# Optimization experiments

Measured on AMD Instinct MI355X. Metric: run time of the kernel, lower is better.

## Reference

```python
import jax, jax.numpy as jnp
import numpy as np

DIM = 192; H = 6; HD = DIM // H; WS = 8; N = WS * WS; B = 2048; NW = 64
SCALE = HD ** -0.5


def _rel_idx():
    # replicates torch meshgrid (indexing='ij') relative position index
    coords = np.stack(np.meshgrid(np.arange(WS), np.arange(WS), indexing='ij'))  # [2,WS,WS]
    flat = coords.reshape(2, -1)  # [2, N]
    rel = flat[:, :, None] - flat[:, None, :]  # [2, N, N]
    rel = rel.transpose(1, 2, 0).astype(np.int64)
    rel[..., 0] += WS - 1
    rel[..., 1] += WS - 1
    rel[..., 0] *= 2 * WS - 1
    return jnp.asarray(rel.sum(-1), dtype=jnp.int32)  # [N, N]


def setup_inputs() -> dict:
    key = jax.random.key(0)
    ks = jax.random.split(key, 8)
    x1 = jax.random.normal(ks[0], (B, N, DIM), jnp.float32)
    x2 = jax.random.normal(ks[1], (B, N, DIM), jnp.float32)
    mask = jnp.zeros((NW, N, N), jnp.float32)
    qw = jax.random.normal(ks[2], (DIM, DIM), jnp.float32) * 0.02
    qb = jnp.zeros((DIM,), jnp.float32)
    kvw = jax.random.normal(ks[3], (2 * DIM, DIM), jnp.float32) * 0.02
    kvb = jnp.zeros((2 * DIM,), jnp.float32)
    rpb = jax.random.normal(ks[4], ((2 * WS - 1) * (2 * WS - 1), H), jnp.float32) * 0.02
    gamma = jnp.full((1,), 0.5, jnp.float32)  # nonzero to exercise LAM path
    pw = jax.random.normal(ks[5], (DIM, DIM), jnp.float32) * 0.02
    pb = jnp.zeros((DIM,), jnp.float32)
    rel_idx = _rel_idx()
    return {"x1": x1, "x2": x2, "mask": mask, "qw": qw, "qb": qb, "kvw": kvw,
            "kvb": kvb, "rpb": rpb, "gamma": gamma, "pw": pw, "pb": pb,
            "rel_idx": rel_idx}


def reference(x1, x2, mask, qw, qb, kvw, kvb, rpb, gamma, pw, pb, rel_idx):
    # q projection -> [B, H, N, HD], pre-scaled (torch code reassigns q = q*scale)
    q = (x1 @ qw.T + qb).reshape(B, N, H, HD).transpose(0, 2, 1, 3) * SCALE
    kv = (x2 @ kvw.T + kvb).reshape(B, N, 2, H, HD)
    k = kv[:, :, 0].transpose(0, 2, 1, 3)  # [B, H, N, HD]
    v = kv[:, :, 1].transpose(0, 2, 1, 3)
    attn = jnp.einsum('bhnd,bhmd->bhnm', q, k)  # [B, H, N, N]
    # gathered relative position bias [H, N, N]
    bias = rpb[rel_idx.reshape(-1)].reshape(N, N, H).transpose(2, 0, 1)
    attn = attn + bias[None]
    attn = attn.reshape(B // NW, NW, H, N, N) + mask[None, :, None]
    attn = jax.nn.softmax(attn.reshape(B, H, N, N), axis=-1)
    y = jnp.einsum('bhnm,bhmd->bhnd', attn, v)  # [B, H, N, HD]
    # LAM module: channel-wise (dim) attention over (head*num)
    xp = y.transpose(0, 3, 1, 2)              # [B, HD, H, N]
    flat = xp.reshape(B, HD, H * N)
    energy = jnp.einsum('bik,bjk->bij', flat, flat)  # [B, HD, HD]
    # note: original computes energy_new but softmaxes raw energy; replicate
    att = jax.nn.softmax(energy, axis=-1)
    out = jnp.einsum('bij,bjk->bik', att, flat).reshape(B, HD, H, N)
    out = gamma * out + xp
    lam = out.transpose(0, 2, 3, 1)            # [B, H, N, HD]
    x = (lam.transpose(0, 2, 1, 3).reshape(B, N, DIM)
         + q.transpose(0, 2, 1, 3).reshape(B, N, DIM)
         + x1)
    return x @ pw.T + pb
```

## Files before the change

### kernel.cpp

```cpp
#include <hip/hip_runtime.h>

#define DIM 192
#define NTOK 64
#define NHEAD 6
#define HDIM 32
#define SCALE 0.17677669529663687f

typedef __attribute__((ext_vector_type(8))) short bf16x8;
typedef __attribute__((ext_vector_type(4))) float f32x4;

__device__ __forceinline__ ushort f2bf(float f) {
    union { float f; unsigned u; } x; x.f = f;
    unsigned r = x.u + 0x7FFFu + ((x.u >> 16) & 1u);
    return (ushort)(r >> 16);
}
__device__ __forceinline__ float bf2f(ushort h) {
    union { unsigned u; float f; } x; x.u = ((unsigned)h) << 16;
    return x.f;
}

__device__ __forceinline__ f32x4 MF(bf16x8 a, bf16x8 b, f32x4 c) {
    return __builtin_amdgcn_mfma_f32_16x16x32_bf16(a, b, c, 0, 0, 0);
}

__device__ __forceinline__ bf16x8 frag(const ushort* base, int stride, int r0, int k0) {
    const int l = threadIdx.x & 63;
    return *(const bf16x8*)(base + (r0 + (l & 15)) * stride + (k0 + ((l >> 4) << 3)));
}

__global__ void prep_weights(const float* __restrict__ qw, const float* __restrict__ kvw,
                             const float* __restrict__ pw, ushort* __restrict__ wbf) {
    int i = blockIdx.x * 256 + threadIdx.x;
    if (i < 36864) wbf[i] = f2bf(qw[i]);
    else if (i < 110592) wbf[i] = f2bf(kvw[i - 36864]);
    else if (i < 147456) wbf[i] = f2bf(pw[i - 110592]);
}

__global__ void prep_cmb(const float* __restrict__ rpb, const float* __restrict__ mask,
                         ushort* __restrict__ cmb) {
    int t = blockIdx.x * 256 + threadIdx.x;
    int e = t << 2;
    int n0 = e & 63;
    int m  = (e >> 6) & 63;
    int hw = e >> 12;
    int h = hw % 6, w = hw / 6;
#pragma unroll
    for (int j = 0; j < 4; ++j) {
        int n = n0 + j;
        int ridx = ((n >> 3) - (m >> 3) + 7) * 15 + ((n & 7) - (m & 7) + 7);
        float v = rpb[ridx * 6 + h] + mask[(w * 64 + n) * 64 + m];
        cmb[e + j] = f2bf(v);
    }
}

__global__ __launch_bounds__(256, 3) void proj_qkv(
    const float* __restrict__ x1, const float* __restrict__ x2,
    const float* __restrict__ qb, const float* __restrict__ kvb,
    const ushort* __restrict__ qwbf, const ushort* __restrict__ kvwbf,
    ushort* __restrict__ Qf, ushort* __restrict__ Kf, ushort* __restrict__ Vf)
{
    __shared__ __align__(16) ushort sXA[64 * 200];
    __shared__ __align__(16) ushort stg[4 * 2560];
    const int tid = threadIdx.x, wave = tid >> 6, lane = tid & 63;
    const int g = lane >> 4, mcol = lane & 15;
    const int b = blockIdx.x >> 1;
    const int kind = blockIdx.x & 1;
    ushort* st = stg + wave * 2560;

    {
        const float4* src = (const float4*)((kind ? x1 : x2) + (size_t)b * 12288);
        for (int i = tid; i < 3072; i += 256) {
            float4 v = src[i];
            int e = i << 2; int n = e / DIM; int c = e - n * DIM;
            ushort4 w;
            ((ushort*)&w)[0] = f2bf(v.x); ((ushort*)&w)[1] = f2bf(v.y);
            ((ushort*)&w)[2] = f2bf(v.z); ((ushort*)&w)[3] = f2bf(v.w);
            *(ushort4*)(&sXA[n * 200 + c]) = w;
        }
    }
    __syncthreads();

    if (kind == 0) {
        for (int t = wave; t < 12; t += 4) {
            const int isV = (t >= 6) ? 1 : 0;
            const int h = isV ? (t - 6) : t;
            bf16x8 wf[2][6];
#pragma unroll
            for (int c2 = 0; c2 < 2; ++c2) {
                int ctg = (isV ? (12 + 2 * h) : (2 * h)) + c2;
#pragma unroll
                for (int ks = 0; ks < 6; ++ks)
                    wf[c2][ks] = frag(kvwbf, DIM, ctg * 16, ks * 32);
            }
            f32x4 acc[4][2];
#pragma unroll
            for (int rt = 0; rt < 4; ++rt)
#pragma unroll
                for (int c2 = 0; c2 < 2; ++c2) acc[rt][c2] = (f32x4){0.f, 0.f, 0.f, 0.f};
#pragma unroll
            for (int rt = 0; rt < 4; ++rt) {
                bf16x8 af[6];
#pragma unroll
                for (int ks = 0; ks < 6; ++ks) af[ks] = frag(sXA, 200, rt * 16, ks * 32);
#pragma unroll
                for (int c2 = 0; c2 < 2; ++c2)
#pragma unroll
                    for (int ks = 0; ks < 6; ++ks)
                        acc[rt][c2] = MF(af[ks], wf[c2][ks], acc[rt][c2]);
            }
            if (!isV) {
#pragma unroll
                for (int c2 = 0; c2 < 2; ++c2) {
                    float bv = kvb[h * 32 + c2 * 16 + mcol];
#pragma unroll
                    for (int rt = 0; rt < 4; ++rt)
#pragma unroll
                        for (int j = 0; j < 4; ++j)
                            st[(rt * 16 + (g << 2) + j) * 40 + c2 * 16 + mcol] = f2bf(acc[rt][c2][j] + bv);
                }
                asm volatile("s_waitcnt lgkmcnt(0)" ::: "memory");
#pragma unroll
                for (int ct = 0; ct < 4; ++ct) {
                    bf16x8 fr = frag(st, 40, ct * 16, 0);
                    *(bf16x8*)(Kf + ((size_t)(b * 6 + h) * 4 + ct) * 512 + lane * 8) = fr;
                }
                asm volatile("s_waitcnt lgkmcnt(0)" ::: "memory");
            } else {
#pragma unroll
                for (int c2 = 0; c2 < 2; ++c2) {
                    float bv = kvb[192 + h * 32 + c2 * 16 + mcol];
#pragma unroll
                    for (int rt = 0; rt < 4; ++rt) {
                        ushort4 w4;
#pragma unroll
                        for (int j = 0; j < 4; ++j) ((ushort*)&w4)[j] = f2bf(acc[rt][c2][j] + bv);
                        *(ushort4*)(&st[(c2 * 16 + mcol) * 72 + rt * 16 + (g << 2)]) = w4;
                    }
                }
                asm volatile("s_waitcnt lgkmcnt(0)" ::: "memory");
#pragma unroll
                for (int c = 0; c < 2; ++c)
#pragma unroll
                    for (int ctd = 0; ctd < 2; ++ctd) {
                        bf16x8 fr = frag(st, 72, ctd * 16, c * 32);
                        *(bf16x8*)(Vf + (((size_t)(b * 6 + h) * 2 + c) * 2 + ctd) * 512 + lane * 8) = fr;
                    }
                asm volatile("s_waitcnt lgkmcnt(0)" ::: "memory");
            }
        }
    } else {
        for (int t = wave; t < 6; t += 4) {
            const int h = t;
            bf16x8 wf[2][6];
#pragma unroll
            for (int c2 = 0; c2 < 2; ++c2)
#pragma unroll
                for (int ks = 0; ks < 6; ++ks)
                    wf[c2][ks] = frag(qwbf, DIM, (2 * h + c2) * 16, ks * 32);
            f32x4 acc[4][2];
#pragma unroll
            for (int rt = 0; rt < 4; ++rt)
#pragma unroll
                for (int c2 = 0; c2 < 2; ++c2) acc[rt][c2] = (f32x4){0.f, 0.f, 0.f, 0.f};
#pragma unroll
            for (int rt = 0; rt < 4; ++rt) {
                bf16x8 af[6];
#pragma unroll
                for (int ks = 0; ks < 6; ++ks) af[ks] = frag(sXA, 200, rt * 16, ks * 32);
#pragma unroll
                for (int c2 = 0; c2 < 2; ++c2)
#pragma unroll
                    for (int ks = 0; ks < 6; ++ks)
                        acc[rt][c2] = MF(af[ks], wf[c2][ks], acc[rt][c2]);
            }
#pragma unroll
            for (int c2 = 0; c2 < 2; ++c2) {
                float bv = qb[h * 32 + c2 * 16 + mcol];
#pragma unroll
                for (int rt = 0; rt < 4; ++rt)
#pragma unroll
                    for (int j = 0; j < 4; ++j)
                        st[(rt * 16 + (g << 2) + j) * 40 + c2 * 16 + mcol] =
                            f2bf((acc[rt][c2][j] + bv) * SCALE);
            }
            asm volatile("s_waitcnt lgkmcnt(0)" ::: "memory");
#pragma unroll
            for (int rt = 0; rt < 4; ++rt) {
                bf16x8 fr = frag(st, 40, rt * 16, 0);
                *(bf16x8*)(Qf + ((size_t)(b * 6 + h) * 4 + rt) * 512 + lane * 8) = fr;
            }
            asm volatile("s_waitcnt lgkmcnt(0)" ::: "memory");
        }
    }
}

__global__ __launch_bounds__(256, 4) void attn_heads(
    const ushort* __restrict__ Qf, ushort* KfY,
    const ushort* __restrict__ Vf, const ushort* __restrict__ cmb)
{
    __shared__ __align__(16) ushort sP[4 * 1280];
    const int tid = threadIdx.x, wave = tid >> 6, lane = tid & 63;
    const int g = lane >> 4, mcol = lane & 15;
    const int gid = blockIdx.x * 4 + wave;
    const int w = gid / 6, h = gid - 6 * (gid / 6);
    const f32x4 zero4 = {0.f, 0.f, 0.f, 0.f};

    const ushort* qp = Qf  + (size_t)gid * 2048;
    ushort*       kp = KfY + (size_t)gid * 2048;
    const ushort* vp = Vf  + (size_t)gid * 2048;
    const ushort* cp = cmb + (size_t)((w & 63) * 6 + h) * 4096;
    ushort* slot = sP + wave * 1280;

    bf16x8 kb[4], vb[4];
#pragma unroll
    for (int ct = 0; ct < 4; ++ct) kb[ct] = *(const bf16x8*)(kp + ct * 512 + lane * 8);
#pragma unroll
    for (int c = 0; c < 4; ++c) vb[c] = *(const bf16x8*)(vp + c * 512 + lane * 8);

    ushort4 y4[4][2];
#pragma unroll
    for (int rt = 0; rt < 4; ++rt) {
        bf16x8 qa = *(const bf16x8*)(qp + rt * 512 + lane * 8);
        f32x4 acc[4];
#pragma unroll
        for (int ct = 0; ct < 4; ++ct) acc[ct] = MF(qa, kb[ct], zero4);
#pragma unroll
        for (int ct = 0; ct < 4; ++ct) {
            ushort4 b4 = *(const ushort4*)(cp + (ct * 16 + mcol) * 64 + rt * 16 + (g << 2));
#pragma unroll
            for (int j = 0; j < 4; ++j) acc[ct][j] += bf2f(((ushort*)&b4)[j]);
        }
        float sm[4];
#pragma unroll
        for (int j = 0; j < 4; ++j) {
            float v = fmaxf(fmaxf(acc[0][j], acc[1][j]), fmaxf(acc[2][j], acc[3][j]));
            v = fmaxf(v, __shfl_xor(v, 1, 64));
            v = fmaxf(v, __shfl_xor(v, 2, 64));
            v = fmaxf(v, __shfl_xor(v, 4, 64));
            v = fmaxf(v, __shfl_xor(v, 8, 64));
            float s = 0.f;
#pragma unroll
            for (int ct = 0; ct < 4; ++ct) {
                float p = __expf(acc[ct][j] - v);
                acc[ct][j] = p; s += p;
            }
            s += __shfl_xor(s, 1, 64);
            s += __shfl_xor(s, 2, 64);
            s += __shfl_xor(s, 4, 64);
            s += __shfl_xor(s, 8, 64);
            sm[j] = 1.0f / s;
        }
#pragma unroll
        for (int ct = 0; ct < 4; ++ct)
#pragma unroll
            for (int j = 0; j < 4; ++j)
                slot[((g << 2) + j) * 72 + ct * 16 + mcol] = f2bf(acc[ct][j] * sm[j]);
        asm volatile("s_waitcnt lgkmcnt(0)" ::: "memory");
        f32x4 ay0 = zero4, ay1 = zero4;
#pragma unroll
        for (int c = 0; c < 2; ++c) {
            bf16x8 pa = frag(slot, 72, 0, c * 32);
            ay0 = MF(pa, vb[c * 2 + 0], ay0);
            ay1 = MF(pa, vb[c * 2 + 1], ay1);
        }
        asm volatile("s_waitcnt lgkmcnt(0)" ::: "memory");
#pragma unroll
        for (int j = 0; j < 4; ++j) {
            ((ushort*)&y4[rt][0])[j] = f2bf(ay0[j]);
            ((ushort*)&y4[rt][1])[j] = f2bf(ay1[j]);
        }
    }
#pragma unroll
    for (int rt = 0; rt < 4; ++rt)
#pragma unroll
        for (int ctd = 0; ctd < 2; ++ctd)
            *(ushort4*)(kp + (ctd * 16 + mcol) * 64 + rt * 16 + (g << 2)) = y4[rt][ctd];
}

__global__ __launch_bounds__(256, 4) void lam_proj(
    const ushort* __restrict__ Yd, const ushort* __restrict__ Qf,
    const float* __restrict__ x1, const float* __restrict__ gammap,
    const ushort* __restrict__ pwbf, const float* __restrict__ pb,
    float* __restrict__ out)
{
    __shared__ __align__(16) ushort sYF[13824];
    __shared__ __align__(16) float  sE[32 * 33];
    __shared__ __align__(16) ushort sAtt[32 * 40];

    const int tid = threadIdx.x, wave = tid >> 6, lane = tid & 63;
    const int g = lane >> 4, mcol = lane & 15;
    const int b = blockIdx.x;
    const float gamma = gammap[0];
    const f32x4 zero4 = {0.f, 0.f, 0.f, 0.f};

    {
        const ushort* src = Yd + (size_t)b * 12288;
        for (int i = tid; i < 3072; i += 256) {
            int hd = i >> 9;
            int rem = i & 511;
            int row = rem >> 4, k4 = rem & 15;
            ushort4 v = *(const ushort4*)(src + hd * 2048 + row * 64 + k4 * 4);
            *(ushort4*)(&sYF[hd * 2304 + row * 72 + k4 * 4]) = v;
        }
    }
    __syncthreads();

    {
        int rt = wave >> 1, ct = wave & 1;
        f32x4 a0 = zero4, a1 = zero4;
#pragma unroll
        for (int hd = 0; hd < 6; hd += 2) {
            const ushort* Y0 = sYF + hd * 2304;
            const ushort* Y1 = sYF + (hd + 1) * 2304;
#pragma unroll
            for (int kk = 0; kk < 2; ++kk) {
                a0 = MF(frag(Y0, 72, rt * 16, kk * 32), frag(Y0, 72, ct * 16, kk * 32), a0);
                a1 = MF(frag(Y1, 72, rt * 16, kk * 32), frag(Y1, 72, ct * 16, kk * 32), a1);
            }
        }
        f32x4 acc = a0 + a1;
#pragma unroll
        for (int j = 0; j < 4; ++j)
            sE[(rt * 16 + (g << 2) + j) * 33 + ct * 16 + mcol] = acc[j];
    }
    __syncthreads();

    {
        int r = tid >> 3, l8 = tid & 7;
        float e[4];
        float mx = -1e30f;
#pragma unroll
        for (int k = 0; k < 4; ++k) { e[k] = sE[r * 33 + l8 + k * 8]; mx = fmaxf(mx, e[k]); }
        mx = fmaxf(mx, __shfl_xor(mx, 1, 64));
        mx = fmaxf(mx, __shfl_xor(mx, 2, 64));
        mx = fmaxf(mx, __shfl_xor(mx, 4, 64));
        float s = 0.f;
#pragma unroll
        for (int k = 0; k < 4; ++k) { e[k] = __expf(e[k] - mx); s += e[k]; }
        s += __shfl_xor(s, 1, 64);
        s += __shfl_xor(s, 2, 64);
        s += __shfl_xor(s, 4, 64);
        float rs = 1.0f / s;
#pragma unroll
        for (int k = 0; k < 4; ++k) sAtt[r * 40 + l8 + k * 8] = f2bf(e[k] * rs);
    }
    __syncthreads();

    ushort4 w4st[12];
#pragma unroll
    for (int i = 0; i < 12; ++i) {
        int t = wave + i * 4;
        int rtL = t & 1, ct = t >> 1;
        int col = ct * 16 + mcol;
        int hh = col >> 6, nn = col & 63;
        const ushort* Yh = sYF + hh * 2304;
        bf16x8 aa = frag(sAtt, 40, rtL * 16, 0);
        bf16x8 bb;
#pragma unroll
        for (int jj = 0; jj < 8; ++jj) bb[jj] = (short)Yh[((g << 3) + jj) * 72 + nn];
        f32x4 acc = MF(aa, bb, zero4);
        int d0 = rtL * 16 + (g << 2);
        ushort4 qv4 = *(const ushort4*)(Qf + (size_t)(b * 6 + hh) * 2048 +
                                        (nn >> 4) * 512 + ((nn & 15) + ((d0 >> 3) << 4)) * 8 + (d0 & 7));
        float4 xv4 = *(const float4*)(x1 + (size_t)b * 12288 + nn * 192 + hh * 32 + d0);
        ushort4 w4;
#pragma unroll
        for (int j = 0; j < 4; ++j) {
            float flatv = bf2f(Yh[(d0 + j) * 72 + nn]);
            float val = gamma * acc[j] + flatv + bf2f(((ushort*)&qv4)[j]) + ((const float*)&xv4)[j];
            ((ushort*)&w4)[j] = f2bf(val);
        }
        w4st[i] = w4;
    }
    __syncthreads();
#pragma unroll
    for (int i = 0; i < 12; ++i) {
        int t = wave + i * 4;
        int rtL = t & 1, ct = t >> 1;
        int col = ct * 16 + mcol;
        int hh = col >> 6, nn = col & 63;
        int d0 = rtL * 16 + (g << 2);
        *(ushort4*)(&sYF[nn * 200 + hh * 32 + d0]) = w4st[i];
    }
    __syncthreads();

    {
        float* outp = out + (size_t)b * 12288;
        const int rt = wave;
        bf16x8 af[6];
#pragma unroll
        for (int ks = 0; ks < 6; ++ks) af[ks] = frag(sYF, 200, rt * 16, ks * 32);
        for (int ct = 0; ct < 12; ++ct) {
            f32x4 acc = zero4;
#pragma unroll
            for (int ks = 0; ks < 6; ++ks)
                acc = MF(af[ks], frag(pwbf, DIM, ct * 16, ks * 32), acc);
            int co = ct * 16 + mcol;
            float pbv = pb[co];
#pragma unroll
            for (int j = 0; j < 4; ++j)
                outp[(rt * 16 + (g << 2) + j) * DIM + co] = acc[j] + pbv;
        }
    }
}

extern "C" void kernel_launch(void* const* d_in, const int* in_sizes, int n_in,
                              void* d_out, int out_size, void* d_ws, size_t ws_size,
                              hipStream_t stream) {
    const float* x1    = (const float*)d_in[0];
    const float* x2    = (const float*)d_in[1];
    const float* mask  = (const float*)d_in[2];
    const float* qw    = (const float*)d_in[3];
    const float* qbv   = (const float*)d_in[4];
    const float* kvw   = (const float*)d_in[5];
    const float* kvbv  = (const float*)d_in[6];
    const float* rpb   = (const float*)d_in[7];
    const float* gamma = (const float*)d_in[8];
    const float* pw    = (const float*)d_in[9];
    const float* pbv   = (const float*)d_in[10];
    ushort* wbf = (ushort*)d_ws;

    prep_weights<<<576, 256, 0, stream>>>(qw, kvw, pw, wbf);

    ushort* cmb = wbf + 147456;
    ushort* Qf  = wbf + 1720320;
    ushort* Kf  = wbf + 26886144;
    ushort* Vf  = wbf + 52051968;
    prep_cmb<<<1536, 256, 0, stream>>>(rpb, mask, cmb);
    proj_qkv<<<4096, 256, 0, stream>>>(x1, x2, qbv, kvbv,
                                       wbf, wbf + 36864, Qf, Kf, Vf);
    attn_heads<<<3072, 256, 0, stream>>>(Qf, Kf, Vf, cmb);
    lam_proj<<<2048, 256, 0, stream>>>(Kf, Qf, x1, gamma,
                                       wbf + 110592, pbv, (float*)d_out);
}
```

Baseline: 296.6 us.

## Switch Q/KV intermediates to row-major layout and tile projection over two batches

```diff
diff --git a/kernel.cpp b/kernel.cpp
--- a/kernel.cpp
+++ b/kernel.cpp
@@ -53,174 +53,120 @@
     }
 }
 
-__global__ __launch_bounds__(256, 3) void proj_qkv(
+__global__ __launch_bounds__(256, 3) void proj2(
     const float* __restrict__ x1, const float* __restrict__ x2,
     const float* __restrict__ qb, const float* __restrict__ kvb,
     const ushort* __restrict__ qwbf, const ushort* __restrict__ kvwbf,
-    ushort* __restrict__ Qf, ushort* __restrict__ Kf, ushort* __restrict__ Vf)
+    ushort* __restrict__ Qb, ushort* __restrict__ KVb)
 {
-    __shared__ __align__(16) ushort sXA[64 * 200];
-    __shared__ __align__(16) ushort stg[4 * 2560];
+    __shared__ __align__(16) ushort sX[128 * 200];
     const int tid = threadIdx.x, wave = tid >> 6, lane = tid & 63;
     const int g = lane >> 4, mcol = lane & 15;
-    const int b = blockIdx.x >> 1;
-    const int kind = blockIdx.x & 1;
-    ushort* st = stg + wave * 2560;
-
-    {
-        const float4* src = (const float4*)((kind ? x1 : x2) + (size_t)b * 12288);
-        for (int i = tid; i < 3072; i += 256) {
+    const int isQ = (blockIdx.x >= 1024);
+    const int grp = isQ ? (blockIdx.x - 1024) : blockIdx.x;
+    const f32x4 zero4 = {0.f, 0.f, 0.f, 0.f};
+
+    {
+        const float4* src = (const float4*)((isQ ? x1 : x2) + (size_t)grp * 24576);
+        for (int i = tid; i < 6144; i += 256) {
             float4 v = src[i];
             int e = i << 2; int n = e / DIM; int c = e - n * DIM;
             ushort4 w;
             ((ushort*)&w)[0] = f2bf(v.x); ((ushort*)&w)[1] = f2bf(v.y);
             ((ushort*)&w)[2] = f2bf(v.z); ((ushort*)&w)[3] = f2bf(v.w);
-            *(ushort4*)(&sXA[n * 200 + c]) = w;
-        }
-    }
-    __syncthreads();
-
-    if (kind == 0) {
-        for (int t = wave; t < 12; t += 4) {
-            const int isV = (t >= 6) ? 1 : 0;
-            const int h = isV ? (t - 6) : t;
-            bf16x8 wf[2][6];
-#pragma unroll
-            for (int c2 = 0; c2 < 2; ++c2) {
-                int ctg = (isV ? (12 + 2 * h) : (2 * h)) + c2;
+            *(ushort4*)(&sX[n * 200 + c]) = w;
+        }
+    }
+    __syncthreads();
+
+    const size_t grow = (size_t)grp * 128;
+    if (!isQ) {
+        for (int q = 0; q < 6; ++q) {
+            int ct = wave * 6 + q;
+            bf16x8 wf[6];
+#pragma unroll
+            for (int ks = 0; ks < 6; ++ks) wf[ks] = frag(kvwbf, DIM, ct * 16, ks * 32);
+            int co = ct * 16 + mcol;
+            float bv = kvb[co];
+            for (int rt = 0; rt < 8; ++rt) {
+                f32x4 acc = zero4;
 #pragma unroll
                 for (int ks = 0; ks < 6; ++ks)
-                    wf[c2][ks] = frag(kvwbf, DIM, ctg * 16, ks * 32);
+                    acc = MF(frag(sX, 200, rt * 16, ks * 32), wf[ks], acc);
+#pragma unroll
+                for (int j = 0; j < 4; ++j)
+                    KVb[(grow + rt * 16 + (g << 2) + j) * 384 + co] = f2bf(acc[j] + bv);
             }
-            f32x4 acc[4][2];
-#pragma unroll
-            for (int rt = 0; rt < 4; ++rt)
-#pragma unroll
-                for (int c2 = 0; c2 < 2; ++c2) acc[rt][c2] = (f32x4){0.f, 0.f, 0.f, 0.f};
-#pragma unroll
-            for (int rt = 0; rt < 4; ++rt) {
-                bf16x8 af[6];
-#pragma unroll
-                for (int ks = 0; ks < 6; ++ks) af[ks] = frag(sXA, 200, rt * 16, ks * 32);
-#pragma unroll
-                for (int c2 = 0; c2 < 2; ++c2)
-#pragma unroll
-                    for (int ks = 0; ks < 6; ++ks)
-                        acc[rt][c2] = MF(af[ks], wf[c2][ks], acc[rt][c2]);
+        }
+    } else {
+        for (int q = 0; q < 3; ++q) {
+            int ct = wave * 3 + q;
+            bf16x8 wf[6];
+#pragma unroll
+            for (int ks = 0; ks < 6; ++ks) wf[ks] = frag(qwbf, DIM, ct * 16, ks * 32);
+            int co = ct * 16 + mcol;
+            float bv = qb[co];
+            for (int rt = 0; rt < 8; ++rt) {
+                f32x4 acc = zero4;
+#pragma unroll
+                for (int ks = 0; ks < 6; ++ks)
+                    acc = MF(frag(sX, 200, rt * 16, ks * 32), wf[ks], acc);
+#pragma unroll
+                for (int j = 0; j < 4; ++j)
+                    Qb[(grow + rt * 16 + (g << 2) + j) * DIM + co] = f2bf((acc[j] + bv) * SCALE);
             }
-            if (!isV) {
-#pragma unroll
-                for (int c2 = 0; c2 < 2; ++c2) {
-                    float bv = kvb[h * 32 + c2 * 16 + mcol];
-#pragma unroll
-                    for (int rt = 0; rt < 4; ++rt)
-#pragma unroll
-                        for (int j = 0; j < 4; ++j)
-                            st[(rt * 16 + (g << 2) + j) * 40 + c2 * 16 + mcol] = f2bf(acc[rt][c2][j] + bv);
-                }
-                asm volatile("s_waitcnt lgkmcnt(0)" ::: "memory");
-#pragma unroll
-                for (int ct = 0; ct < 4; ++ct) {
-                    bf16x8 fr = frag(st, 40, ct * 16, 0);
-                    *(bf16x8*)(Kf + ((size_t)(b * 6 + h) * 4 + ct) * 512 + lane * 8) = fr;
-                }
-                asm volatile("s_waitcnt lgkmcnt(0)" ::: "memory");
-            } else {
-#pragma unroll
-                for (int c2 = 0; c2 < 2; ++c2) {
-                    float bv = kvb[192 + h * 32 + c2 * 16 + mcol];
-#pragma unroll
-                    for (int rt = 0; rt < 4; ++rt) {
-                        ushort4 w4;
-#pragma unroll
-                        for (int j = 0; j < 4; ++j) ((ushort*)&w4)[j] = f2bf(acc[rt][c2][j] + bv);
-                        *(ushort4*)(&st[(c2 * 16 + mcol) * 72 + rt * 16 + (g << 2)]) = w4;
-                    }
-                }
-                asm volatile("s_waitcnt lgkmcnt(0)" ::: "memory");
-#pragma unroll
-                for (int c = 0; c < 2; ++c)
-#pragma unroll
-                    for (int ctd = 0; ctd < 2; ++ctd) {
-                        bf16x8 fr = frag(st, 72, ctd * 16, c * 32);
-                        *(bf16x8*)(Vf + (((size_t)(b * 6 + h) * 2 + c) * 2 + ctd) * 512 + lane * 8) = fr;
-                    }
-                asm volatile("s_waitcnt lgkmcnt(0)" ::: "memory");
-            }
-        }
-    } else {
-        for (int t = wave; t < 6; t += 4) {
-            const int h = t;
-            bf16x8 wf[2][6];
-#pragma unroll
-            for (int c2 = 0; c2 < 2; ++c2)
-#pragma unroll
-                for (int ks = 0; ks < 6; ++ks)
-                    wf[c2][ks] = frag(qwbf, DIM, (2 * h + c2) * 16, ks * 32);
-            f32x4 acc[4][2];
-#pragma unroll
-            for (int rt = 0; rt < 4; ++rt)
-#pragma unroll
-                for (int c2 = 0; c2 < 2; ++c2) acc[rt][c2] = (f32x4){0.f, 0.f, 0.f, 0.f};
-#pragma unroll
-            for (int rt = 0; rt < 4; ++rt) {
-                bf16x8 af[6];
-#pragma unroll
-                for (int ks = 0; ks < 6; ++ks) af[ks] = frag(sXA, 200, rt * 16, ks * 32);
-#pragma unroll
-                for (int c2 = 0; c2 < 2; ++c2)
-#pragma unroll
-                    for (int ks = 0; ks < 6; ++ks)
-                        acc[rt][c2] = MF(af[ks], wf[c2][ks], acc[rt][c2]);
-            }
-#pragma unroll
-            for (int c2 = 0; c2 < 2; ++c2) {
-                float bv = qb[h * 32 + c2 * 16 + mcol];
-#pragma unroll
-                for (int rt = 0; rt < 4; ++rt)
-#pragma unroll
-                    for (int j = 0; j < 4; ++j)
-                        st[(rt * 16 + (g << 2) + j) * 40 + c2 * 16 + mcol] =
-                            f2bf((acc[rt][c2][j] + bv) * SCALE);
-            }
-            asm volatile("s_waitcnt lgkmcnt(0)" ::: "memory");
-#pragma unroll
-            for (int rt = 0; rt < 4; ++rt) {
-                bf16x8 fr = frag(st, 40, rt * 16, 0);
-                *(bf16x8*)(Qf + ((size_t)(b * 6 + h) * 4 + rt) * 512 + lane * 8) = fr;
-            }
-            asm volatile("s_waitcnt lgkmcnt(0)" ::: "memory");
-        }
-    }
-}
-
-__global__ __launch_bounds__(256, 4) void attn_heads(
-    const ushort* __restrict__ Qf, ushort* KfY,
-    const ushort* __restrict__ Vf, const ushort* __restrict__ cmb)
+        }
+    }
+}
+
+__global__ __launch_bounds__(256, 5) void attn_heads(
+    const ushort* __restrict__ Qb, ushort* __restrict__ KVb,
+    const ushort* __restrict__ cmb)
 {
     __shared__ __align__(16) ushort sP[4 * 1280];
+    __shared__ __align__(16) ushort sV[4 * 2176];
     const int tid = threadIdx.x, wave = tid >> 6, lane = tid & 63;
     const int g = lane >> 4, mcol = lane & 15;
     const int gid = blockIdx.x * 4 + wave;
     const int w = gid / 6, h = gid - 6 * (gid / 6);
     const f32x4 zero4 = {0.f, 0.f, 0.f, 0.f};
 
-    const ushort* qp = Qf  + (size_t)gid * 2048;
-    ushort*       kp = KfY + (size_t)gid * 2048;
-    const ushort* vp = Vf  + (size_t)gid * 2048;
+    const ushort* qp = Qb + (size_t)w * 12288 + h * 32;
+    ushort*       kp = KVb + (size_t)w * 24576 + h * 32;
+    const ushort* vp = kp + 192;
     const ushort* cp = cmb + (size_t)((w & 63) * 6 + h) * 4096;
-    ushort* slot = sP + wave * 1280;
-
-    bf16x8 kb[4], vb[4];
-#pragma unroll
-    for (int ct = 0; ct < 4; ++ct) kb[ct] = *(const bf16x8*)(kp + ct * 512 + lane * 8);
-#pragma unroll
-    for (int c = 0; c < 4; ++c) vb[c] = *(const bf16x8*)(vp + c * 512 + lane * 8);
-
-    ushort4 y4[4][2];
+    ushort* slotP = sP + wave * 1280;
+    ushort* slotV = sV + wave * 2176;
+
+    bf16x8 kb[4];
+#pragma unroll
+    for (int ct = 0; ct < 4; ++ct) kb[ct] = frag(kp, 384, ct * 16, 0);
+
+#pragma unroll
+    for (int it = 0; it < 8; ++it) {
+        int i = (it << 6) + lane;
+        int row = i >> 3, c4 = i & 7;
+        ushort4 v4 = *(const ushort4*)(vp + row * 384 + (c4 << 2));
+        int ba = row * 34 + (c4 << 2);
+        slotV[ba + 0] = v4.x; slotV[ba + 1] = v4.y;
+        slotV[ba + 2] = v4.z; slotV[ba + 3] = v4.w;
+    }
+    asm volatile("s_waitcnt lgkmcnt(0)" ::: "memory");
+    bf16x8 vb[4];
+#pragma unroll
+    for (int c = 0; c < 2; ++c)
+#pragma unroll
+        for (int ctd = 0; ctd < 2; ++ctd) {
+            bf16x8 t;
+#pragma unroll
+            for (int j = 0; j < 8; ++j)
+                t[j] = (short)slotV[(c * 32 + (g << 3) + j) * 34 + ctd * 16 + mcol];
+            vb[c * 2 + ctd] = t;
+        }
+
 #pragma unroll
     for (int rt = 0; rt < 4; ++rt) {
-        bf16x8 qa = *(const bf16x8*)(qp + rt * 512 + lane * 8);
+        bf16x8 qa = frag(qp, DIM, rt * 16, 0);
         f32x4 acc[4];
 #pragma unroll
         for (int ct = 0; ct < 4; ++ct) acc[ct] = MF(qa, kb[ct], zero4);
@@ -254,31 +200,27 @@
         for (int ct = 0; ct < 4; ++ct)
 #pragma unroll
             for (int j = 0; j < 4; ++j)
-                slot[((g << 2) + j) * 72 + ct * 16 + mcol] = f2bf(acc[ct][j] * sm[j]);
+                slotP[((g << 2) + j) * 72 + ct * 16 + mcol] = f2bf(acc[ct][j] * sm[j]);
         asm volatile("s_waitcnt lgkmcnt(0)" ::: "memory");
         f32x4 ay0 = zero4, ay1 = zero4;
 #pragma unroll
         for (int c = 0; c < 2; ++c) {
-            bf16x8 pa = frag(slot, 72, 0, c * 32);
+            bf16x8 pa = frag(slotP, 72, 0, c * 32);
             ay0 = MF(pa, vb[c * 2 + 0], ay0);
             ay1 = MF(pa, vb[c * 2 + 1], ay1);
         }
         asm volatile("s_waitcnt lgkmcnt(0)" ::: "memory");
 #pragma unroll
         for (int j = 0; j < 4; ++j) {
-            ((ushort*)&y4[rt][0])[j] = f2bf(ay0[j]);
-            ((ushort*)&y4[rt][1])[j] = f2bf(ay1[j]);
-        }
-    }
-#pragma unroll
-    for (int rt = 0; rt < 4; ++rt)
-#pragma unroll
-        for (int ctd = 0; ctd < 2; ++ctd)
-            *(ushort4*)(kp + (ctd * 16 + mcol) * 64 + rt * 16 + (g << 2)) = y4[rt][ctd];
+            int n = rt * 16 + (g << 2) + j;
+            kp[n * 384 + mcol]      = f2bf(ay0[j]);
+            kp[n * 384 + 16 + mcol] = f2bf(ay1[j]);
+        }
+    }
 }
 
 __global__ __launch_bounds__(256, 4) void lam_proj(
-    const ushort* __restrict__ Yd, const ushort* __restrict__ Qf,
+    const ushort* __restrict__ KVb, const ushort* __restrict__ Qb,
     const float* __restrict__ x1, const float* __restrict__ gammap,
     const ushort* __restrict__ pwbf, const float* __restrict__ pb,
     float* __restrict__ out)
@@ -294,13 +236,13 @@
     const f32x4 zero4 = {0.f, 0.f, 0.f, 0.f};
 
     {
-        const ushort* src = Yd + (size_t)b * 12288;
+        const ushort* src = KVb + (size_t)b * 24576;
         for (int i = tid; i < 3072; i += 256) {
-            int hd = i >> 9;
-            int rem = i & 511;
-            int row = rem >> 4, k4 = rem & 15;
-            ushort4 v = *(const ushort4*)(src + hd * 2048 + row * 64 + k4 * 4);
-            *(ushort4*)(&sYF[hd * 2304 + row * 72 + k4 * 4]) = v;
+            int seg = i >> 3, c4 = i & 7;
+            int hd = seg % 6, n = seg / 6;
+            ushort4 v4 = *(const ushort4*)(src + n * 384 + hd * 32 + (c4 << 2));
+            int ba = hd * 2304 + (c4 << 2) * 72 + n;
+            sYF[ba] = v4.x; sYF[ba + 72] = v4.y; sYF[ba + 144] = v4.z; sYF[ba + 216] = v4.w;
         }
     }
     __syncthreads();
@@ -360,8 +302,7 @@
         for (int jj = 0; jj < 8; ++jj) bb[jj] = (short)Yh[((g << 3) + jj) * 72 + nn];
         f32x4 acc = MF(aa, bb, zero4);
         int d0 = rtL * 16 + (g << 2);
-        ushort4 qv4 = *(const ushort4*)(Qf + (size_t)(b * 6 + hh) * 2048 +
-                                        (nn >> 4) * 512 + ((nn & 15) + ((d0 >> 3) << 4)) * 8 + (d0 & 7));
+        ushort4 qv4 = *(const ushort4*)(Qb + (size_t)(b * 64 + nn) * DIM + hh * 32 + d0);
         float4 xv4 = *(const float4*)(x1 + (size_t)b * 12288 + nn * 192 + hh * 32 + d0);
         ushort4 w4;
 #pragma unroll
@@ -423,13 +364,12 @@
     prep_weights<<<576, 256, 0, stream>>>(qw, kvw, pw, wbf);
 
     ushort* cmb = wbf + 147456;
-    ushort* Qf  = wbf + 1720320;
-    ushort* Kf  = wbf + 26886144;
-    ushort* Vf  = wbf + 52051968;
+    ushort* Qb  = wbf + 1720320;
+    ushort* KVb = wbf + 26886144;
     prep_cmb<<<1536, 256, 0, stream>>>(rpb, mask, cmb);
-    proj_qkv<<<4096, 256, 0, stream>>>(x1, x2, qbv, kvbv,
-                                       wbf, wbf + 36864, Qf, Kf, Vf);
-    attn_heads<<<3072, 256, 0, stream>>>(Qf, Kf, Vf, cmb);
-    lam_proj<<<2048, 256, 0, stream>>>(Kf, Qf, x1, gamma,
+    proj2<<<2048, 256, 0, stream>>>(x1, x2, qbv, kvbv,
+                                    wbf, wbf + 36864, Qb, KVb);
+    attn_heads<<<3072, 256, 0, stream>>>(Qb, KVb, cmb);
+    lam_proj<<<2048, 256, 0, stream>>>(KVb, Qb, x1, gamma,
                                        wbf + 110592, pbv, (float*)d_out);
 }
```

After: 572.2 us. +92.9%, slower.

## Merge Q and KV projection blocks and load activations directly into registers

Applied to the files above, without the earlier changes.

```diff
diff --git a/kernel.cpp b/kernel.cpp
--- a/kernel.cpp
+++ b/kernel.cpp
@@ -53,126 +53,65 @@
     }
 }
 
-__global__ __launch_bounds__(256, 3) void proj_qkv(
+__global__ __launch_bounds__(384, 3) void proj4(
     const float* __restrict__ x1, const float* __restrict__ x2,
     const float* __restrict__ qb, const float* __restrict__ kvb,
     const ushort* __restrict__ qwbf, const ushort* __restrict__ kvwbf,
     ushort* __restrict__ Qf, ushort* __restrict__ Kf, ushort* __restrict__ Vf)
 {
-    __shared__ __align__(16) ushort sXA[64 * 200];
-    __shared__ __align__(16) ushort stg[4 * 2560];
+    __shared__ __align__(16) ushort stg6[6 * 2560];
     const int tid = threadIdx.x, wave = tid >> 6, lane = tid & 63;
     const int g = lane >> 4, mcol = lane & 15;
-    const int b = blockIdx.x >> 1;
-    const int kind = blockIdx.x & 1;
-    ushort* st = stg + wave * 2560;
-
-    {
-        const float4* src = (const float4*)((kind ? x1 : x2) + (size_t)b * 12288);
-        for (int i = tid; i < 3072; i += 256) {
-            float4 v = src[i];
-            int e = i << 2; int n = e / DIM; int c = e - n * DIM;
-            ushort4 w;
-            ((ushort*)&w)[0] = f2bf(v.x); ((ushort*)&w)[1] = f2bf(v.y);
-            ((ushort*)&w)[2] = f2bf(v.z); ((ushort*)&w)[3] = f2bf(v.w);
-            *(ushort4*)(&sXA[n * 200 + c]) = w;
-        }
-    }
-    __syncthreads();
-
-    if (kind == 0) {
-        for (int t = wave; t < 12; t += 4) {
-            const int isV = (t >= 6) ? 1 : 0;
-            const int h = isV ? (t - 6) : t;
-            bf16x8 wf[2][6];
-#pragma unroll
-            for (int c2 = 0; c2 < 2; ++c2) {
-                int ctg = (isV ? (12 + 2 * h) : (2 * h)) + c2;
+    const int b = blockIdx.x;
+    const f32x4 zero4 = {0.f, 0.f, 0.f, 0.f};
+    ushort* st = stg6 + wave * 2560;
+
+    const int isQ = (wave >= 4);
+    const float* xp = (isQ ? x1 : x2) + (size_t)b * 12288;
+
+    for (int q = 0; q < 3; ++q) {
+        const int t = (isQ ? (wave - 4) : wave) * 3 + q;
+        const int isV = (!isQ && t >= 6);
+        const int h = isQ ? t : (isV ? t - 6 : t);
+        const ushort* wmat = isQ ? qwbf : kvwbf;
+        const int rowbase = (isV ? 192 : 0) + h * 32;
+
+        bf16x8 wf[2][6];
+#pragma unroll
+        for (int c2 = 0; c2 < 2; ++c2)
+#pragma unroll
+            for (int ks = 0; ks < 6; ++ks)
+                wf[c2][ks] = frag(wmat, DIM, rowbase + c2 * 16, ks * 32);
+
+        f32x4 acc[4][2];
+#pragma unroll
+        for (int rt = 0; rt < 4; ++rt)
+#pragma unroll
+            for (int c2 = 0; c2 < 2; ++c2) acc[rt][c2] = zero4;
+
+#pragma unroll
+        for (int rt = 0; rt < 4; ++rt) {
+            const float* xr = xp + (rt * 16 + (lane & 15)) * DIM + ((lane >> 4) << 3);
+            bf16x8 af[6];
+#pragma unroll
+            for (int ks = 0; ks < 6; ++ks) {
+                float4 a0 = *(const float4*)(xr + ks * 32);
+                float4 a1 = *(const float4*)(xr + ks * 32 + 4);
+                bf16x8 tv;
+                tv[0] = (short)f2bf(a0.x); tv[1] = (short)f2bf(a0.y);
+                tv[2] = (short)f2bf(a0.z); tv[3] = (short)f2bf(a0.w);
+                tv[4] = (short)f2bf(a1.x); tv[5] = (short)f2bf(a1.y);
+                tv[6] = (short)f2bf(a1.z); tv[7] = (short)f2bf(a1.w);
+                af[ks] = tv;
+            }
+#pragma unroll
+            for (int c2 = 0; c2 < 2; ++c2)
 #pragma unroll
                 for (int ks = 0; ks < 6; ++ks)
-                    wf[c2][ks] = frag(kvwbf, DIM, ctg * 16, ks * 32);
-            }
-            f32x4 acc[4][2];
-#pragma unroll
-            for (int rt = 0; rt < 4; ++rt)
-#pragma unroll
-                for (int c2 = 0; c2 < 2; ++c2) acc[rt][c2] = (f32x4){0.f, 0.f, 0.f, 0.f};
-#pragma unroll
-            for (int rt = 0; rt < 4; ++rt) {
-                bf16x8 af[6];
-#pragma unroll
-                for (int ks = 0; ks < 6; ++ks) af[ks] = frag(sXA, 200, rt * 16, ks * 32);
-#pragma unroll
-                for (int c2 = 0; c2 < 2; ++c2)
-#pragma unroll
-                    for (int ks = 0; ks < 6; ++ks)
-                        acc[rt][c2] = MF(af[ks], wf[c2][ks], acc[rt][c2]);
-            }
-            if (!isV) {
-#pragma unroll
-                for (int c2 = 0; c2 < 2; ++c2) {
-                    float bv = kvb[h * 32 + c2 * 16 + mcol];
-#pragma unroll
-                    for (int rt = 0; rt < 4; ++rt)
-#pragma unroll
-                        for (int j = 0; j < 4; ++j)
-                            st[(rt * 16 + (g << 2) + j) * 40 + c2 * 16 + mcol] = f2bf(acc[rt][c2][j] + bv);
-                }
-                asm volatile("s_waitcnt lgkmcnt(0)" ::: "memory");
-#pragma unroll
-                for (int ct = 0; ct < 4; ++ct) {
-                    bf16x8 fr = frag(st, 40, ct * 16, 0);
-                    *(bf16x8*)(Kf + ((size_t)(b * 6 + h) * 4 + ct) * 512 + lane * 8) = fr;
-                }
-                asm volatile("s_waitcnt lgkmcnt(0)" ::: "memory");
-            } else {
-#pragma unroll
-                for (int c2 = 0; c2 < 2; ++c2) {
-                    float bv = kvb[192 + h * 32 + c2 * 16 + mcol];
-#pragma unroll
-                    for (int rt = 0; rt < 4; ++rt) {
-                        ushort4 w4;
-#pragma unroll
-                        for (int j = 0; j < 4; ++j) ((ushort*)&w4)[j] = f2bf(acc[rt][c2][j] + bv);
-                        *(ushort4*)(&st[(c2 * 16 + mcol) * 72 + rt * 16 + (g << 2)]) = w4;
-                    }
-                }
-                asm volatile("s_waitcnt lgkmcnt(0)" ::: "memory");
-#pragma unroll
-                for (int c = 0; c < 2; ++c)
-#pragma unroll
-                    for (int ctd = 0; ctd < 2; ++ctd) {
-                        bf16x8 fr = frag(st, 72, ctd * 16, c * 32);
-                        *(bf16x8*)(Vf + (((size_t)(b * 6 + h) * 2 + c) * 2 + ctd) * 512 + lane * 8) = fr;
-                    }
-                asm volatile("s_waitcnt lgkmcnt(0)" ::: "memory");
-            }
-        }
-    } else {
-        for (int t = wave; t < 6; t += 4) {
-            const int h = t;
-            bf16x8 wf[2][6];
-#pragma unroll
-            for (int c2 = 0; c2 < 2; ++c2)
-#pragma unroll
-                for (int ks = 0; ks < 6; ++ks)
-                    wf[c2][ks] = frag(qwbf, DIM, (2 * h + c2) * 16, ks * 32);
-            f32x4 acc[4][2];
-#pragma unroll
-            for (int rt = 0; rt < 4; ++rt)
-#pragma unroll
-                for (int c2 = 0; c2 < 2; ++c2) acc[rt][c2] = (f32x4){0.f, 0.f, 0.f, 0.f};
-#pragma unroll
-            for (int rt = 0; rt < 4; ++rt) {
-                bf16x8 af[6];
-#pragma unroll
-                for (int ks = 0; ks < 6; ++ks) af[ks] = frag(sXA, 200, rt * 16, ks * 32);
-#pragma unroll
-                for (int c2 = 0; c2 < 2; ++c2)
-#pragma unroll
-                    for (int ks = 0; ks < 6; ++ks)
-                        acc[rt][c2] = MF(af[ks], wf[c2][ks], acc[rt][c2]);
-            }
+                    acc[rt][c2] = MF(af[ks], wf[c2][ks], acc[rt][c2]);
+        }
+
+        if (isQ) {
 #pragma unroll
             for (int c2 = 0; c2 < 2; ++c2) {
                 float bv = qb[h * 32 + c2 * 16 + mcol];
@@ -189,6 +128,45 @@
                 bf16x8 fr = frag(st, 40, rt * 16, 0);
                 *(bf16x8*)(Qf + ((size_t)(b * 6 + h) * 4 + rt) * 512 + lane * 8) = fr;
             }
+            asm volatile("s_waitcnt lgkmcnt(0)" ::: "memory");
+        } else if (!isV) {
+#pragma unroll
+            for (int c2 = 0; c2 < 2; ++c2) {
+                float bv = kvb[h * 32 + c2 * 16 + mcol];
+#pragma unroll
+                for (int rt = 0; rt < 4; ++rt)
+#pragma unroll
+                    for (int j = 0; j < 4; ++j)
+                        st[(rt * 16 + (g << 2) + j) * 40 + c2 * 16 + mcol] =
+                            f2bf(acc[rt][c2][j] + bv);
+            }
+            asm volatile("s_waitcnt lgkmcnt(0)" ::: "memory");
+#pragma unroll
+            for (int ct = 0; ct < 4; ++ct) {
+                bf16x8 fr = frag(st, 40, ct * 16, 0);
+                *(bf16x8*)(Kf + ((size_t)(b * 6 + h) * 4 + ct) * 512 + lane * 8) = fr;
+            }
+            asm volatile("s_waitcnt lgkmcnt(0)" ::: "memory");
+        } else {
+#pragma unroll
+            for (int c2 = 0; c2 < 2; ++c2) {
+                float bv = kvb[192 + h * 32 + c2 * 16 + mcol];
+#pragma unroll
+                for (int rt = 0; rt < 4; ++rt) {
+                    ushort4 w4;
+#pragma unroll
+                    for (int j = 0; j < 4; ++j) ((ushort*)&w4)[j] = f2bf(acc[rt][c2][j] + bv);
+                    *(ushort4*)(&st[(c2 * 16 + mcol) * 72 + rt * 16 + (g << 2)]) = w4;
+                }
+            }
+            asm volatile("s_waitcnt lgkmcnt(0)" ::: "memory");
+#pragma unroll
+            for (int c = 0; c < 2; ++c)
+#pragma unroll
+                for (int ctd = 0; ctd < 2; ++ctd) {
+                    bf16x8 fr = frag(st, 72, ctd * 16, c * 32);
+                    *(bf16x8*)(Vf + (((size_t)(b * 6 + h) * 2 + c) * 2 + ctd) * 512 + lane * 8) = fr;
+                }
             asm volatile("s_waitcnt lgkmcnt(0)" ::: "memory");
         }
     }
@@ -427,8 +405,8 @@
     ushort* Kf  = wbf + 26886144;
     ushort* Vf  = wbf + 52051968;
     prep_cmb<<<1536, 256, 0, stream>>>(rpb, mask, cmb);
-    proj_qkv<<<4096, 256, 0, stream>>>(x1, x2, qbv, kvbv,
-                                       wbf, wbf + 36864, Qf, Kf, Vf);
+    proj4<<<2048, 384, 0, stream>>>(x1, x2, qbv, kvbv,
+                                    wbf, wbf + 36864, Qf, Kf, Vf);
     attn_heads<<<3072, 256, 0, stream>>>(Qf, Kf, Vf, cmb);
     lam_proj<<<2048, 256, 0, stream>>>(Kf, Qf, x1, gamma,
                                        wbf + 110592, pbv, (float*)d_out);
```

Result: slower. 316.3 us (+6.7%).

## Merge Q and KV projection blocks into one block per batch with smaller staging

Applied to the files above, without the earlier changes.

```diff
diff --git a/kernel.cpp b/kernel.cpp
--- a/kernel.cpp
+++ b/kernel.cpp
@@ -53,22 +53,22 @@
     }
 }
 
-__global__ __launch_bounds__(256, 3) void proj_qkv(
+__global__ __launch_bounds__(256, 4) void proj7(
     const float* __restrict__ x1, const float* __restrict__ x2,
     const float* __restrict__ qb, const float* __restrict__ kvb,
     const ushort* __restrict__ qwbf, const ushort* __restrict__ kvwbf,
     ushort* __restrict__ Qf, ushort* __restrict__ Kf, ushort* __restrict__ Vf)
 {
     __shared__ __align__(16) ushort sXA[64 * 200];
-    __shared__ __align__(16) ushort stg[4 * 2560];
+    __shared__ __align__(16) ushort stg[4 * 1280];
     const int tid = threadIdx.x, wave = tid >> 6, lane = tid & 63;
     const int g = lane >> 4, mcol = lane & 15;
-    const int b = blockIdx.x >> 1;
-    const int kind = blockIdx.x & 1;
-    ushort* st = stg + wave * 2560;
-
-    {
-        const float4* src = (const float4*)((kind ? x1 : x2) + (size_t)b * 12288);
+    const int b = blockIdx.x;
+    const f32x4 zero4 = {0.f, 0.f, 0.f, 0.f};
+    ushort* st = stg + wave * 1280;
+
+    {
+        const float4* src = (const float4*)(x2 + (size_t)b * 12288);
         for (int i = tid; i < 3072; i += 256) {
             float4 v = src[i];
             int e = i << 2; int n = e / DIM; int c = e - n * DIM;
@@ -80,114 +80,135 @@
     }
     __syncthreads();
 
-    if (kind == 0) {
-        for (int t = wave; t < 12; t += 4) {
-            const int isV = (t >= 6) ? 1 : 0;
-            const int h = isV ? (t - 6) : t;
-            bf16x8 wf[2][6];
-#pragma unroll
-            for (int c2 = 0; c2 < 2; ++c2) {
-                int ctg = (isV ? (12 + 2 * h) : (2 * h)) + c2;
+    for (int t = wave; t < 12; t += 4) {
+        const int isV = (t >= 6) ? 1 : 0;
+        const int h = isV ? (t - 6) : t;
+        bf16x8 wf[2][6];
+#pragma unroll
+        for (int c2 = 0; c2 < 2; ++c2) {
+            int ctg = (isV ? (12 + 2 * h) : (2 * h)) + c2;
+#pragma unroll
+            for (int ks = 0; ks < 6; ++ks)
+                wf[c2][ks] = frag(kvwbf, DIM, ctg * 16, ks * 32);
+        }
+        f32x4 acc[4][2];
+#pragma unroll
+        for (int rt = 0; rt < 4; ++rt)
+#pragma unroll
+            for (int c2 = 0; c2 < 2; ++c2) acc[rt][c2] = zero4;
+#pragma unroll
+        for (int rt = 0; rt < 4; ++rt) {
+            bf16x8 af[6];
+#pragma unroll
+            for (int ks = 0; ks < 6; ++ks) af[ks] = frag(sXA, 200, rt * 16, ks * 32);
+#pragma unroll
+            for (int c2 = 0; c2 < 2; ++c2)
 #pragma unroll
                 for (int ks = 0; ks < 6; ++ks)
-                    wf[c2][ks] = frag(kvwbf, DIM, ctg * 16, ks * 32);
-            }
-            f32x4 acc[4][2];
-#pragma unroll
-            for (int rt = 0; rt < 4; ++rt)
-#pragma unroll
-                for (int c2 = 0; c2 < 2; ++c2) acc[rt][c2] = (f32x4){0.f, 0.f, 0.f, 0.f};
-#pragma unroll
-            for (int rt = 0; rt < 4; ++rt) {
-                bf16x8 af[6];
-#pragma unroll
-                for (int ks = 0; ks < 6; ++ks) af[ks] = frag(sXA, 200, rt * 16, ks * 32);
-#pragma unroll
-                for (int c2 = 0; c2 < 2; ++c2)
-#pragma unroll
-                    for (int ks = 0; ks < 6; ++ks)
-                        acc[rt][c2] = MF(af[ks], wf[c2][ks], acc[rt][c2]);
-            }
-            if (!isV) {
+                    acc[rt][c2] = MF(af[ks], wf[c2][ks], acc[rt][c2]);
+        }
+        if (!isV) {
+#pragma unroll
+            for (int ph = 0; ph < 2; ++ph) {
 #pragma unroll
                 for (int c2 = 0; c2 < 2; ++c2) {
                     float bv = kvb[h * 32 + c2 * 16 + mcol];
 #pragma unroll
-                    for (int rt = 0; rt < 4; ++rt)
+                    for (int rl = 0; rl < 2; ++rl)
 #pragma unroll
                         for (int j = 0; j < 4; ++j)
-                            st[(rt * 16 + (g << 2) + j) * 40 + c2 * 16 + mcol] = f2bf(acc[rt][c2][j] + bv);
+                            st[(rl * 16 + (g << 2) + j) * 40 + c2 * 16 + mcol] =
+                                f2bf(acc[2 * ph + rl][c2][j] + bv);
                 }
                 asm volatile("s_waitcnt lgkmcnt(0)" ::: "memory");
 #pragma unroll
-                for (int ct = 0; ct < 4; ++ct) {
-                    bf16x8 fr = frag(st, 40, ct * 16, 0);
-                    *(bf16x8*)(Kf + ((size_t)(b * 6 + h) * 4 + ct) * 512 + lane * 8) = fr;
+                for (int cl = 0; cl < 2; ++cl) {
+                    bf16x8 fr = frag(st, 40, cl * 16, 0);
+                    *(bf16x8*)(Kf + ((size_t)(b * 6 + h) * 4 + 2 * ph + cl) * 512 + lane * 8) = fr;
                 }
                 asm volatile("s_waitcnt lgkmcnt(0)" ::: "memory");
-            } else {
+            }
+        } else {
+#pragma unroll
+            for (int c = 0; c < 2; ++c) {
 #pragma unroll
                 for (int c2 = 0; c2 < 2; ++c2) {
                     float bv = kvb[192 + h * 32 + c2 * 16 + mcol];
 #pragma unroll
-                    for (int rt = 0; rt < 4; ++rt) {
+                    for (int rl = 0; rl < 2; ++rl) {
                         ushort4 w4;
 #pragma unroll
-                        for (int j = 0; j < 4; ++j) ((ushort*)&w4)[j] = f2bf(acc[rt][c2][j] + bv);
-                        *(ushort4*)(&st[(c2 * 16 + mcol) * 72 + rt * 16 + (g << 2)]) = w4;
+                        for (int j = 0; j < 4; ++j)
+                            ((ushort*)&w4)[j] = f2bf(acc[2 * c + rl][c2][j] + bv);
+                        *(ushort4*)(&st[(c2 * 16 + mcol) * 40 + rl * 16 + (g << 2)]) = w4;
                     }
                 }
                 asm volatile("s_waitcnt lgkmcnt(0)" ::: "memory");
 #pragma unroll
-                for (int c = 0; c < 2; ++c)
-#pragma unroll
-                    for (int ctd = 0; ctd < 2; ++ctd) {
-                        bf16x8 fr = frag(st, 72, ctd * 16, c * 32);
-                        *(bf16x8*)(Vf + (((size_t)(b * 6 + h) * 2 + c) * 2 + ctd) * 512 + lane * 8) = fr;
-                    }
+                for (int ctd = 0; ctd < 2; ++ctd) {
+                    bf16x8 fr = frag(st, 40, ctd * 16, 0);
+                    *(bf16x8*)(Vf + (((size_t)(b * 6 + h) * 2 + c) * 2 + ctd) * 512 + lane * 8) = fr;
+                }
                 asm volatile("s_waitcnt lgkmcnt(0)" ::: "memory");
             }
         }
-    } else {
-        for (int t = wave; t < 6; t += 4) {
-            const int h = t;
-            bf16x8 wf[2][6];
+    }
+    __syncthreads();
+
+    {
+        const float4* src = (const float4*)(x1 + (size_t)b * 12288);
+        for (int i = tid; i < 3072; i += 256) {
+            float4 v = src[i];
+            int e = i << 2; int n = e / DIM; int c = e - n * DIM;
+            ushort4 w;
+            ((ushort*)&w)[0] = f2bf(v.x); ((ushort*)&w)[1] = f2bf(v.y);
+            ((ushort*)&w)[2] = f2bf(v.z); ((ushort*)&w)[3] = f2bf(v.w);
+            *(ushort4*)(&sXA[n * 200 + c]) = w;
+        }
+    }
+    __syncthreads();
+
+    for (int t = wave; t < 6; t += 4) {
+        const int h = t;
+        bf16x8 wf[2][6];
+#pragma unroll
+        for (int c2 = 0; c2 < 2; ++c2)
+#pragma unroll
+            for (int ks = 0; ks < 6; ++ks)
+                wf[c2][ks] = frag(qwbf, DIM, (2 * h + c2) * 16, ks * 32);
+        f32x4 acc[4][2];
+#pragma unroll
+        for (int rt = 0; rt < 4; ++rt)
+#pragma unroll
+            for (int c2 = 0; c2 < 2; ++c2) acc[rt][c2] = zero4;
+#pragma unroll
+        for (int rt = 0; rt < 4; ++rt) {
+            bf16x8 af[6];
+#pragma unroll
+            for (int ks = 0; ks < 6; ++ks) af[ks] = frag(sXA, 200, rt * 16, ks * 32);
 #pragma unroll
             for (int c2 = 0; c2 < 2; ++c2)
 #pragma unroll
                 for (int ks = 0; ks < 6; ++ks)
-                    wf[c2][ks] = frag(qwbf, DIM, (2 * h + c2) * 16, ks * 32);
-            f32x4 acc[4][2];
-#pragma unroll
-            for (int rt = 0; rt < 4; ++rt)
-#pragma unroll
-                for (int c2 = 0; c2 < 2; ++c2) acc[rt][c2] = (f32x4){0.f, 0.f, 0.f, 0.f};
-#pragma unroll
-            for (int rt = 0; rt < 4; ++rt) {
-                bf16x8 af[6];
-#pragma unroll
-                for (int ks = 0; ks < 6; ++ks) af[ks] = frag(sXA, 200, rt * 16, ks * 32);
-#pragma unroll
-                for (int c2 = 0; c2 < 2; ++c2)
-#pragma unroll
-                    for (int ks = 0; ks < 6; ++ks)
-                        acc[rt][c2] = MF(af[ks], wf[c2][ks], acc[rt][c2]);
-            }
+                    acc[rt][c2] = MF(af[ks], wf[c2][ks], acc[rt][c2]);
+        }
+#pragma unroll
+        for (int ph = 0; ph < 2; ++ph) {
 #pragma unroll
             for (int c2 = 0; c2 < 2; ++c2) {
                 float bv = qb[h * 32 + c2 * 16 + mcol];
 #pragma unroll
-                for (int rt = 0; rt < 4; ++rt)
+                for (int rl = 0; rl < 2; ++rl)
 #pragma unroll
                     for (int j = 0; j < 4; ++j)
-                        st[(rt * 16 + (g << 2) + j) * 40 + c2 * 16 + mcol] =
-                            f2bf((acc[rt][c2][j] + bv) * SCALE);
+                        st[(rl * 16 + (g << 2) + j) * 40 + c2 * 16 + mcol] =
+                            f2bf((acc[2 * ph + rl][c2][j] + bv) * SCALE);
             }
             asm volatile("s_waitcnt lgkmcnt(0)" ::: "memory");
 #pragma unroll
-            for (int rt = 0; rt < 4; ++rt) {
-                bf16x8 fr = frag(st, 40, rt * 16, 0);
-                *(bf16x8*)(Qf + ((size_t)(b * 6 + h) * 4 + rt) * 512 + lane * 8) = fr;
+            for (int cl = 0; cl < 2; ++cl) {
+                bf16x8 fr = frag(st, 40, cl * 16, 0);
+                *(bf16x8*)(Qf + ((size_t)(b * 6 + h) * 4 + 2 * ph + cl) * 512 + lane * 8) = fr;
             }
             asm volatile("s_waitcnt lgkmcnt(0)" ::: "memory");
         }
@@ -427,8 +448,8 @@
     ushort* Kf  = wbf + 26886144;
     ushort* Vf  = wbf + 52051968;
     prep_cmb<<<1536, 256, 0, stream>>>(rpb, mask, cmb);
-    proj_qkv<<<4096, 256, 0, stream>>>(x1, x2, qbv, kvbv,
-                                       wbf, wbf + 36864, Qf, Kf, Vf);
+    proj7<<<2048, 256, 0, stream>>>(x1, x2, qbv, kvbv,
+                                    wbf, wbf + 36864, Qf, Kf, Vf);
     attn_heads<<<3072, 256, 0, stream>>>(Qf, Kf, Vf, cmb);
     lam_proj<<<2048, 256, 0, stream>>>(Kf, Qf, x1, gamma,
                                        wbf + 110592, pbv, (float*)d_out);
```

Measured after the change: 274.0 us. -7.6%, faster.
